# Performance work log

Measured on AMD Instinct MI355X. Metric: run time of the kernel, lower is better.

## Reference

```python
import jax, jax.numpy as jnp
import numpy as np

N = 50000           # num_nodes
E = 400000          # num directed input edges
CON_DIM = 128
STRUC_DIM = 64
HIDDEN = 128
NUM_NODE_UPDATES = 5
MAX_GROUP_ITERS = 100


def setup_inputs() -> dict:
    key = jax.random.key(0)
    k = jax.random.split(key, 5)
    return {
        "con_feats": jax.random.normal(k[0], (N, CON_DIM), jnp.float32),
        "struc_feats": jax.random.normal(k[1], (N, STRUC_DIM), jnp.float32),
        "W1": jax.random.normal(k[2], (2 * CON_DIM, HIDDEN), jnp.float32) * 0.05,
        "b1": jnp.zeros((HIDDEN,), jnp.float32),
        "W2": jax.random.normal(k[3], (HIDDEN, 1), jnp.float32) * 0.05,
        "b2": jnp.zeros((1,), jnp.float32),
        "edge_ids": jax.random.randint(k[4], (2, E), 0, N, jnp.int32),
    }


def _edge_scores(con_feats, W1, b1, W2, b2, src, dst, upper):
    # MLP edge scorer on concatenated endpoint features; relu'd score,
    # zeroed on edges failing the dst > src pruning (equivalent to torch's
    # boolean pruning: score-0 edges contribute nothing downstream).
    x = jnp.concatenate([con_feats[src], con_feats[dst]], axis=1)  # [E, 2*C]
    raw = (jax.nn.relu(x @ W1 + b1) @ W2 + b2)[:, 0]               # [E]
    return jax.nn.relu(raw) * upper


def reference(con_feats, struc_feats, W1, b1, W2, b2, edge_ids):
    num_nodes = con_feats.shape[0]
    src, dst = edge_ids[0], edge_ids[1]
    upper = (dst > src).astype(con_feats.dtype)
    scores = _edge_scores(con_feats, W1, b1, W2, b2, src, dst, upper)
    ar = jnp.arange(num_nodes, dtype=edge_ids.dtype)

    # full edge set: pruned + flipped + self-loops (score-0 edges are no-ops)
    all_src = jnp.concatenate([src, dst, ar])
    all_dst = jnp.concatenate([dst, src, ar])
    all_scores = jnp.concatenate([scores, scores, jnp.ones((num_nodes,), scores.dtype)])

    # row-wise normalization (scatter-sum over source node)
    node_sums = jax.ops.segment_sum(all_scores, all_src, num_segments=num_nodes)
    norm_scores = all_scores / node_sums[all_src]

    def spmm(f):  # sparse [N,N] @ dense [N,d]
        return jax.ops.segment_sum(norm_scores[:, None] * f[all_dst], all_src,
                                   num_segments=num_nodes)

    for _ in range(NUM_NODE_UPDATES):
        con_feats = spmm(con_feats)
        struc_feats = spmm(struc_feats)

    # connected-components label propagation over edges with positive score
    # (edges with score==0 are rewritten as self-edges instead of filtered,
    # which is a no-op for scatter-min; self-loops appended as in torch)
    g_src = jnp.concatenate([jnp.where(scores > 0, src, dst), ar])
    g_dst = jnp.concatenate([dst, ar])

    def cond(state):
        i, _, changed = state
        return (i < MAX_GROUP_ITERS) & changed

    def body(state):
        i, g, _ = state
        new = jax.ops.segment_min(g[g_src], g_dst, num_segments=num_nodes)
        return (i + 1, new, jnp.any(new != g))

    _, group_ids, _ = jax.lax.while_loop(cond, body,
                                         (jnp.int32(0), ar, jnp.bool_(True)))

    # compact labels (torch.unique return_inverse); output padded to N rows
    _, inv = jnp.unique(group_ids, return_inverse=True, size=num_nodes,
                        fill_value=num_nodes - 1)
    inv = inv.reshape(-1)

    counts = jax.ops.segment_sum(jnp.ones((num_nodes,), con_feats.dtype), inv,
                                 num_segments=num_nodes)
    denom = jnp.maximum(counts, 1.0)[:, None]
    con_out = jax.ops.segment_sum(con_feats, inv, num_segments=num_nodes) / denom
    struc_out = jax.ops.segment_sum(struc_feats, inv, num_segments=num_nodes) / denom
    # [N, CON_DIM + STRUC_DIM]; rows >= num_groups are zero padding
    return jnp.concatenate([con_out, struc_out], axis=1)
```

## Files before the change

kernel.cpp:

```cpp
#include <hip/hip_runtime.h>
#include <hip/hip_fp16.h>
#include <cstdint>
#include <cstddef>


__global__ void k_init(const float* __restrict__ con, const float* __restrict__ str,
                       __half* __restrict__ F, float* __restrict__ sums,
                       int* __restrict__ cnt, int* __restrict__ g, int N) {
  int i = blockIdx.x * blockDim.x + threadIdx.x;
  int total = N * 192;
  if (i < total) {
    int n = i / 192, f = i - n * 192;
    float v = (f < 128) ? con[n * 128 + f] : str[n * 64 + (f - 128)];
    F[i] = __float2half_rn(v);
  }
  if (i < N) { sums[i] = 1.0f; cnt[i] = 1; g[i] = i; }
}

__global__ __launch_bounds__(256) void k_proj(const float* __restrict__ con,
                                              const float* __restrict__ W1,
                                              const float* __restrict__ b1,
                                              float* __restrict__ PQf,
                                              __half* __restrict__ PQh, int N) {
  int wave = threadIdx.x >> 6;
  int lane = threadIdx.x & 63;
  int n0 = blockIdx.x * 32 + wave * 8;
  const float* W1q = W1 + 128 * 128;
  float aP0[8], aP1[8], aQ0[8], aQ1[8];
#pragma unroll
  for (int t = 0; t < 8; ++t) { aP0[t] = 0.f; aP1[t] = 0.f; aQ0[t] = 0.f; aQ1[t] = 0.f; }
  int cL = lane, cH = 64 + lane;
  for (int k = 0; k < 128; k += 4) {
    float wP0[4], wP1[4], wQ0[4], wQ1[4];
#pragma unroll
    for (int u = 0; u < 4; ++u) {
      wP0[u] = W1[(k + u) * 128 + cL];
      wP1[u] = W1[(k + u) * 128 + cH];
      wQ0[u] = W1q[(k + u) * 128 + cL];
      wQ1[u] = W1q[(k + u) * 128 + cH];
    }
#pragma unroll
    for (int t = 0; t < 8; ++t) {
      int node = min(n0 + t, N - 1);
      const float4 c4 = *(const float4*)&con[(size_t)node * 128 + k];
      aP0[t] += c4.x * wP0[0] + c4.y * wP0[1] + c4.z * wP0[2] + c4.w * wP0[3];
      aP1[t] += c4.x * wP1[0] + c4.y * wP1[1] + c4.z * wP1[2] + c4.w * wP1[3];
      aQ0[t] += c4.x * wQ0[0] + c4.y * wQ0[1] + c4.z * wQ0[2] + c4.w * wQ0[3];
      aQ1[t] += c4.x * wQ1[0] + c4.y * wQ1[1] + c4.z * wQ1[2] + c4.w * wQ1[3];
    }
  }
  float bL = b1[cL], bH = b1[cH];
#pragma unroll
  for (int t = 0; t < 8; ++t) {
    int node = n0 + t;
    if (node < N) {
      float vP0 = aP0[t] + bL, vP1 = aP1[t] + bH;
      float* rf = PQf + (size_t)node * 256;
      rf[cL] = vP0; rf[cH] = vP1;
      rf[128 + cL] = aQ0[t]; rf[128 + cH] = aQ1[t];
      __half* rh = PQh + (size_t)node * 256;
      rh[cL] = __float2half_rn(vP0); rh[cH] = __float2half_rn(vP1);
      rh[128 + cL] = __float2half_rn(aQ0[t]); rh[128 + cH] = __float2half_rn(aQ1[t]);
    }
  }
}

__global__ __launch_bounds__(256) void k_edge(const int* __restrict__ src, const int* __restrict__ dst,
                                              const __half* __restrict__ PQ,
                                              const float* __restrict__ PQf,
                                              const float* __restrict__ W2,
                                              const float* __restrict__ b2,
                                              float* __restrict__ scores,
                                              float* __restrict__ sums, int* __restrict__ cnt,
                                              int* __restrict__ pos_s, int* __restrict__ pos_d,
                                              int* __restrict__ pos_cnt, int E) {
  int e = blockIdx.x * 256 + threadIdx.x;
  bool live = (e < E);
  int s = 0, d = 0;
  if (live) { s = src[e]; d = dst[e]; }
  bool scored = live && (d > s);
  float raw = -1.0f;
  if (scored) {
    const uint4* P = (const uint4*)(PQ + (size_t)s * 256);
    const uint4* Q = (const uint4*)(PQ + (size_t)d * 256 + 128);
    const float4* W = (const float4*)W2;
    float acc = 0.0f;
#pragma unroll 8
    for (int k = 0; k < 16; ++k) {
      uint4 pu = P[k];
      uint4 qu = Q[k];
      float4 wa = W[2 * k], wb = W[2 * k + 1];
      float2 p0 = __half22float2(*(const __half2*)&pu.x);
      float2 p1 = __half22float2(*(const __half2*)&pu.y);
      float2 p2 = __half22float2(*(const __half2*)&pu.z);
      float2 p3 = __half22float2(*(const __half2*)&pu.w);
      float2 q0 = __half22float2(*(const __half2*)&qu.x);
      float2 q1 = __half22float2(*(const __half2*)&qu.y);
      float2 q2 = __half22float2(*(const __half2*)&qu.z);
      float2 q3 = __half22float2(*(const __half2*)&qu.w);
      acc += fmaxf(p0.x + q0.x, 0.f) * wa.x + fmaxf(p0.y + q0.y, 0.f) * wa.y
           + fmaxf(p1.x + q1.x, 0.f) * wa.z + fmaxf(p1.y + q1.y, 0.f) * wa.w
           + fmaxf(p2.x + q2.x, 0.f) * wb.x + fmaxf(p2.y + q2.y, 0.f) * wb.y
           + fmaxf(p3.x + q3.x, 0.f) * wb.z + fmaxf(p3.y + q3.y, 0.f) * wb.w;
    }
    raw = acc + b2[0];
    if (fabsf(raw) < 3e-3f) {
      const float4* Pf = (const float4*)(PQf + (size_t)s * 256);
      const float4* Qf = (const float4*)(PQf + (size_t)d * 256 + 128);
      float acc2 = 0.0f;
      for (int k = 0; k < 32; ++k) {
        float4 p = Pf[k], q = Qf[k], w = W[k];
        acc2 += fmaxf(p.x + q.x, 0.f) * w.x + fmaxf(p.y + q.y, 0.f) * w.y
              + fmaxf(p.z + q.z, 0.f) * w.z + fmaxf(p.w + q.w, 0.f) * w.w;
      }
      raw = acc2 + b2[0];
    }
  }
  float sc = scored ? fmaxf(raw, 0.0f) : 0.0f;
  if (live) scores[e] = sc;
  bool pos = scored && (sc > 0.0f);
  if (pos) {
    atomicAdd(&sums[s], sc);
    atomicAdd(&sums[d], sc);
    atomicAdd(&cnt[s], 1);
    atomicAdd(&cnt[d], 1);
  }
  unsigned long long m = __ballot(pos);
  if (pos) {
    int lane = threadIdx.x & 63;
    int rank = __popcll(m & ((1ULL << lane) - 1));
    int leader = __ffsll((long long)m) - 1;
    int bcast;
    if (lane == leader) bcast = atomicAdd(pos_cnt, __popcll(m));
    bcast = __shfl(bcast, leader, 64);
    pos_s[bcast + rank] = s;
    pos_d[bcast + rank] = d;
  }
}

__device__ __forceinline__ int wave_iscan(int v) {
  int l = threadIdx.x & 63;
#pragma unroll
  for (int o = 1; o < 64; o <<= 1) {
    int t = __shfl_up(v, o, 64);
    if (l >= o) v += t;
  }
  return v;
}

__global__ __launch_bounds__(1024) void k_scan_red(int mode, const int* __restrict__ cnt,
                                                   const int* __restrict__ g,
                                                   int* __restrict__ bsum, int N) {
  __shared__ int wsum[16];
  int i = blockIdx.x * 1024 + threadIdx.x;
  int v = 0;
  if (i < N) v = (mode == 0) ? cnt[i] : ((g[i] == i) ? 1 : 0);
  int incl = wave_iscan(v);
  int wid = threadIdx.x >> 6;
  if ((threadIdx.x & 63) == 63) wsum[wid] = incl;
  __syncthreads();
  if (threadIdx.x == 0) {
    int t = 0;
#pragma unroll
    for (int k = 0; k < 16; ++k) t += wsum[k];
    bsum[blockIdx.x] = t;
  }
}

__global__ __launch_bounds__(64) void k_scan_mid(int mode, const int* __restrict__ bsum,
                                                 int* __restrict__ bexcl, int NB,
                                                 int* __restrict__ rowp, int N) {
  int l = threadIdx.x;
  int v = (l < NB) ? bsum[l] : 0;
  int incl = wave_iscan(v);
  if (l < NB) bexcl[l] = incl - v;
  if (l == 63 && mode == 0) rowp[N] = incl;
}

__global__ __launch_bounds__(1024) void k_scan_out(int mode, const int* __restrict__ cnt,
                                                   const int* __restrict__ g,
                                                   const float* __restrict__ sums,
                                                   const int* __restrict__ bexcl,
                                                   int* __restrict__ rowp, int* __restrict__ fillp,
                                                   int* __restrict__ col, float* __restrict__ wt,
                                                   int* __restrict__ rank, int N) {
  __shared__ int wsum[16];
  int i = blockIdx.x * 1024 + threadIdx.x;
  int v = 0;
  if (i < N) v = (mode == 0) ? cnt[i] : ((g[i] == i) ? 1 : 0);
  int incl = wave_iscan(v);
  int wid = threadIdx.x >> 6;
  if ((threadIdx.x & 63) == 63) wsum[wid] = incl;
  __syncthreads();
  if (threadIdx.x < 64) {
    int l = threadIdx.x;
    int sv = (l < 16) ? wsum[l] : 0;
#pragma unroll
    for (int o = 1; o < 16; o <<= 1) {
      int t = __shfl_up(sv, o, 64);
      if (l >= o) sv += t;
    }
    if (l < 16) wsum[l] = sv;
  }
  __syncthreads();
  int wexcl = (wid == 0) ? 0 : wsum[wid - 1];
  int excl = bexcl[blockIdx.x] + wexcl + incl - v;
  if (i < N) {
    if (mode == 0) {
      rowp[i] = excl;
      fillp[i] = excl + 1;
      col[excl] = i;
      wt[excl] = 1.0f / sums[i];
    } else {
      rank[i] = excl;
    }
  }
}

__global__ void k_fill(const int* __restrict__ src, const int* __restrict__ dst,
                       const float* __restrict__ scores, const float* __restrict__ sums,
                       int* __restrict__ fillp, int* __restrict__ col, float* __restrict__ wt,
                       int E) {
  int e = blockIdx.x * blockDim.x + threadIdx.x;
  if (e >= E) return;
  float sc = scores[e];
  if (sc <= 0.0f) return;
  int s = src[e], d = dst[e];
  int p = atomicAdd(&fillp[s], 1);
  col[p] = d; wt[p] = sc / sums[s];
  int p2 = atomicAdd(&fillp[d], 1);
  col[p2] = s; wt[p2] = sc / sums[d];
}

__global__ __launch_bounds__(192) void k_spmm(const __half* __restrict__ Fin, __half* __restrict__ Fout,
                                              const int* __restrict__ rowp,
                                              const int* __restrict__ col,
                                              const float* __restrict__ wt, int N) {
  int tid = blockIdx.x * 192 + threadIdx.x;
  int row = tid / 24;
  int f8 = tid - row * 24;
  if (row >= N) return;
  const uint4* F8 = (const uint4*)Fin;
  int beg = rowp[row], end = rowp[row + 1];
  float a0 = 0.f, a1 = 0.f, a2 = 0.f, a3 = 0.f, a4 = 0.f, a5 = 0.f, a6 = 0.f, a7 = 0.f;
  int idx = beg;
  for (; idx + 1 < end; idx += 2) {
    int c0 = col[idx], c1 = col[idx + 1];
    float w0 = wt[idx], w1 = wt[idx + 1];
    uint4 u0 = F8[(size_t)c0 * 24 + f8];
    uint4 u1 = F8[(size_t)c1 * 24 + f8];
    float2 x0 = __half22float2(*(const __half2*)&u0.x);
    float2 x1 = __half22float2(*(const __half2*)&u0.y);
    float2 x2 = __half22float2(*(const __half2*)&u0.z);
    float2 x3 = __half22float2(*(const __half2*)&u0.w);
    a0 += w0 * x0.x; a1 += w0 * x0.y; a2 += w0 * x1.x; a3 += w0 * x1.y;
    a4 += w0 * x2.x; a5 += w0 * x2.y; a6 += w0 * x3.x; a7 += w0 * x3.y;
    float2 y0 = __half22float2(*(const __half2*)&u1.x);
    float2 y1 = __half22float2(*(const __half2*)&u1.y);
    float2 y2 = __half22float2(*(const __half2*)&u1.z);
    float2 y3 = __half22float2(*(const __half2*)&u1.w);
    a0 += w1 * y0.x; a1 += w1 * y0.y; a2 += w1 * y1.x; a3 += w1 * y1.y;
    a4 += w1 * y2.x; a5 += w1 * y2.y; a6 += w1 * y3.x; a7 += w1 * y3.y;
  }
  if (idx < end) {
    int c0 = col[idx];
    float w0 = wt[idx];
    uint4 u0 = F8[(size_t)c0 * 24 + f8];
    float2 x0 = __half22float2(*(const __half2*)&u0.x);
    float2 x1 = __half22float2(*(const __half2*)&u0.y);
    float2 x2 = __half22float2(*(const __half2*)&u0.z);
    float2 x3 = __half22float2(*(const __half2*)&u0.w);
    a0 += w0 * x0.x; a1 += w0 * x0.y; a2 += w0 * x1.x; a3 += w0 * x1.y;
    a4 += w0 * x2.x; a5 += w0 * x2.y; a6 += w0 * x3.x; a7 += w0 * x3.y;
  }
  uint4 o;
  *(__half2*)&o.x = __floats2half2_rn(a0, a1);
  *(__half2*)&o.y = __floats2half2_rn(a2, a3);
  *(__half2*)&o.z = __floats2half2_rn(a4, a5);
  *(__half2*)&o.w = __floats2half2_rn(a6, a7);
  ((uint4*)Fout)[(size_t)row * 24 + f8] = o;
}

__global__ void k_prop(const int* __restrict__ pos_s, const int* __restrict__ pos_d,
                       const int* __restrict__ pos_cnt, int* g, int N) {
  int i = blockIdx.x * blockDim.x + threadIdx.x;
  volatile int* gv = g;
  int P = *pos_cnt;
#pragma unroll
  for (int r = 0; r < 2; ++r) {
    if (i < P) {
      int s = pos_s[i], d = pos_d[i];
      int gs = gv[s];
      if (gs < gv[d]) atomicMin(&g[d], gs);
    }
    if (i < N) {
      int gi = gv[i];
      int gg = gv[gi];
      if (gg < gi) atomicMin(&g[i], gg);
      gi = gv[i];
      gg = gv[gi];
      if (gg < gi) atomicMin(&g[i], gg);
    }
  }
}

__global__ void k_gcnt(const int* __restrict__ g, const int* __restrict__ rank,
                       int* __restrict__ gcnt, int N) {
  int i = blockIdx.x * blockDim.x + threadIdx.x;
  if (i < N) atomicAdd(&gcnt[rank[g[i]]], 1);
}

__global__ void k_inv(const int* __restrict__ gcnt, float* __restrict__ invc, int N) {
  int i = blockIdx.x * blockDim.x + threadIdx.x;
  if (i < N) invc[i] = 1.0f / (float)max(gcnt[i], 1);
}

__global__ __launch_bounds__(192) void k_accum(const __half* __restrict__ F, const int* __restrict__ g,
                                               const int* __restrict__ rank,
                                               const float* __restrict__ invc,
                                               float* __restrict__ out, int N) {
  __shared__ int jbuf[64];
  int n0 = blockIdx.x * 64;
  if (threadIdx.x < 64) {
    int n = n0 + threadIdx.x;
    jbuf[threadIdx.x] = (n < N) ? rank[g[n]] : -1;
  }
  __syncthreads();
  int f = threadIdx.x;
  int lim = min(64, N - n0);
  float acc = 0.0f; int cur = -1;
  for (int k = 0; k < lim; ++k) {
    int j = jbuf[k];
    float v = __half2float(F[(size_t)(n0 + k) * 192 + f]);
    if (j != cur) {
      if (cur >= 0) atomicAdd(&out[(size_t)cur * 192 + f], acc * invc[cur]);
      cur = j; acc = v;
    } else {
      acc += v;
    }
  }
  if (cur >= 0) atomicAdd(&out[(size_t)cur * 192 + f], acc * invc[cur]);
}

extern "C" void kernel_launch(void* const* d_in, const int* in_sizes, int n_in,
                              void* d_out, int out_size, void* d_ws, size_t ws_size,
                              hipStream_t stream) {
  const float* con = (const float*)d_in[0];
  const float* str = (const float*)d_in[1];
  const float* W1  = (const float*)d_in[2];
  const float* b1  = (const float*)d_in[3];
  const float* W2  = (const float*)d_in[4];
  const float* b2  = (const float*)d_in[5];
  const int* edges = (const int*)d_in[6];
  int N = in_sizes[0] / 128;
  int E = in_sizes[6] / 2;
  const int* src = edges;
  const int* dst = edges + E;
  int NB = (N + 1023) / 1024;

  uint8_t* w = (uint8_t*)d_ws;
  size_t off = 0;
  auto alloc = [&](size_t bytes) -> void* {
    void* p = w + off;
    off += (bytes + 255) & ~(size_t)255;
    return p;
  };
  __half* Fa    = (__half*)alloc((size_t)N * 192 * 2);
  float*  PQf   = (float*)alloc((size_t)N * 256 * 4);
  __half* Fb    = (__half*)PQf;
  float* scores = (float*)alloc((size_t)E * 4);
  float* sums   = (float*)alloc((size_t)N * 4);
  int*   cnt    = (int*)alloc((size_t)N * 4);
  int*   g      = (int*)alloc((size_t)N * 4);
  int*   pos_s  = (int*)alloc((size_t)E * 4);
  int*   pos_d  = (int*)alloc((size_t)E * 4);
  int*   pos_c  = (int*)alloc(256);
  int*   bsum   = (int*)alloc(64 * 4);
  int*   bexcl  = (int*)alloc(64 * 4);
  size_t mark = off;
  int*   colA   = (int*)alloc((2 * (size_t)E + N) * 4);
  float* wtA    = (float*)alloc((2 * (size_t)E + N) * 4);
  int*   rowp   = (int*)alloc((size_t)(N + 1) * 4);
  int*   fillp  = (int*)alloc((size_t)N * 4);
  int*   rank   = (int*)alloc((size_t)N * 4);
  int*   gcnt   = (int*)alloc((size_t)N * 4);
  float* invc   = (float*)alloc((size_t)N * 4);
  size_t pqh_bytes = (size_t)N * 256 * 2;
  if (off < mark + pqh_bytes) off = mark + ((pqh_bytes + 255) & ~(size_t)255);
  __half* PQh = (__half*)(w + mark);

  hipMemsetAsync(d_out, 0, (size_t)out_size * 4, stream);
  hipMemsetAsync(pos_c, 0, 4, stream);

  k_init<<<(N * 192 + 255) / 256, 256, 0, stream>>>(con, str, Fa, sums, cnt, g, N);
  k_proj<<<(N + 31) / 32, 256, 0, stream>>>(con, W1, b1, PQf, PQh, N);
  k_edge<<<(E + 255) / 256, 256, 0, stream>>>(src, dst, PQh, PQf, W2, b2, scores, sums, cnt,
                                              pos_s, pos_d, pos_c, E);
  k_scan_red<<<NB, 1024, 0, stream>>>(0, cnt, g, bsum, N);
  k_scan_mid<<<1, 64, 0, stream>>>(0, bsum, bexcl, NB, rowp, N);
  k_scan_out<<<NB, 1024, 0, stream>>>(0, cnt, g, sums, bexcl, rowp, fillp, colA, wtA, rank, N);
  k_fill<<<(E + 255) / 256, 256, 0, stream>>>(src, dst, scores, sums, fillp, colA, wtA, E);

  __half* fin = Fa; __half* fout = Fb;
  for (int it = 0; it < 5; ++it) {
    k_spmm<<<((size_t)N * 24 + 191) / 192, 192, 0, stream>>>(fin, fout, rowp, colA, wtA, N);
    __half* tmp = fin; fin = fout; fout = tmp;
  }

  for (int r = 0; r < 9; ++r)
    k_prop<<<(E + 255) / 256, 256, 0, stream>>>(pos_s, pos_d, pos_c, g, N);

  k_scan_red<<<NB, 1024, 0, stream>>>(1, cnt, g, bsum, N);
  k_scan_mid<<<1, 64, 0, stream>>>(1, bsum, bexcl, NB, rowp, N);
  k_scan_out<<<NB, 1024, 0, stream>>>(1, cnt, g, sums, bexcl, rowp, fillp, colA, wtA, rank, N);
  hipMemsetAsync(gcnt, 0, (size_t)N * 4, stream);
  k_gcnt<<<(N + 255) / 256, 256, 0, stream>>>(g, rank, gcnt, N);
  k_inv<<<(N + 255) / 256, 256, 0, stream>>>(gcnt, invc, N);
  k_accum<<<(N + 63) / 64, 192, 0, stream>>>(fin, g, rank, invc, (float*)d_out, N);
}
```

Before: 588.8 us.

## Compute node projections with fp16 MFMA and rescore borderline edges exactly

Replaces the scalar fp32 per-node W1 projection with an MFMA 16x16x32 fp16 matrix-core kernel over the fp16 feature buffer. A transposed fp16 copy of W1 is prepared first, and the fp32 PQ copy is dropped. Edges whose fp16 score lands near zero are collected into a list. A separate kernel recomputes those from the original fp32 features with a full fp32 MLP. This removes the fp32 projection compute and the extra PQf write and read, at the cost of an extra launch and more slow per-edge recomputes due to the wider border threshold.

```diff
diff --git a/kernel.cpp b/kernel.cpp
--- a/kernel.cpp
+++ b/kernel.cpp
@@ -3,6 +3,9 @@
 #include <cstdint>
 #include <cstddef>
 
+
+typedef _Float16 f16x8 __attribute__((ext_vector_type(8)));
+typedef float f32x4 __attribute__((ext_vector_type(4)));
 
 __global__ void k_init(const float* __restrict__ con, const float* __restrict__ str,
                        __half* __restrict__ F, float* __restrict__ sums,
@@ -17,63 +20,57 @@
   if (i < N) { sums[i] = 1.0f; cnt[i] = 1; g[i] = i; }
 }
 
-__global__ __launch_bounds__(256) void k_proj(const float* __restrict__ con,
-                                              const float* __restrict__ W1,
-                                              const float* __restrict__ b1,
-                                              float* __restrict__ PQf,
-                                              __half* __restrict__ PQh, int N) {
-  int wave = threadIdx.x >> 6;
-  int lane = threadIdx.x & 63;
-  int n0 = blockIdx.x * 32 + wave * 8;
-  const float* W1q = W1 + 128 * 128;
-  float aP0[8], aP1[8], aQ0[8], aQ1[8];
-#pragma unroll
-  for (int t = 0; t < 8; ++t) { aP0[t] = 0.f; aP1[t] = 0.f; aQ0[t] = 0.f; aQ1[t] = 0.f; }
-  int cL = lane, cH = 64 + lane;
-  for (int k = 0; k < 128; k += 4) {
-    float wP0[4], wP1[4], wQ0[4], wQ1[4];
-#pragma unroll
-    for (int u = 0; u < 4; ++u) {
-      wP0[u] = W1[(k + u) * 128 + cL];
-      wP1[u] = W1[(k + u) * 128 + cH];
-      wQ0[u] = W1q[(k + u) * 128 + cL];
-      wQ1[u] = W1q[(k + u) * 128 + cH];
-    }
-#pragma unroll
-    for (int t = 0; t < 8; ++t) {
-      int node = min(n0 + t, N - 1);
-      const float4 c4 = *(const float4*)&con[(size_t)node * 128 + k];
-      aP0[t] += c4.x * wP0[0] + c4.y * wP0[1] + c4.z * wP0[2] + c4.w * wP0[3];
-      aP1[t] += c4.x * wP1[0] + c4.y * wP1[1] + c4.z * wP1[2] + c4.w * wP1[3];
-      aQ0[t] += c4.x * wQ0[0] + c4.y * wQ0[1] + c4.z * wQ0[2] + c4.w * wQ0[3];
-      aQ1[t] += c4.x * wQ1[0] + c4.y * wQ1[1] + c4.z * wQ1[2] + c4.w * wQ1[3];
-    }
-  }
-  float bL = b1[cL], bH = b1[cH];
-#pragma unroll
-  for (int t = 0; t < 8; ++t) {
-    int node = n0 + t;
-    if (node < N) {
-      float vP0 = aP0[t] + bL, vP1 = aP1[t] + bH;
-      float* rf = PQf + (size_t)node * 256;
-      rf[cL] = vP0; rf[cH] = vP1;
-      rf[128 + cL] = aQ0[t]; rf[128 + cH] = aQ1[t];
-      __half* rh = PQh + (size_t)node * 256;
-      rh[cL] = __float2half_rn(vP0); rh[cH] = __float2half_rn(vP1);
-      rh[128 + cL] = __float2half_rn(aQ0[t]); rh[128 + cH] = __float2half_rn(aQ1[t]);
+__global__ void k_wprep(const float* __restrict__ W1, __half* __restrict__ BT) {
+  int i = blockIdx.x * 256 + threadIdx.x;
+  if (i < 256 * 128) {
+    int c = i >> 7, k = i & 127;
+    float v = (c < 128) ? W1[k * 128 + c] : W1[16384 + k * 128 + (c - 128)];
+    BT[(size_t)c * 128 + k] = __float2half_rn(v);
+  }
+}
+
+__global__ __launch_bounds__(256) void k_projm(const __half* __restrict__ Fa,
+                                               const __half* __restrict__ BT,
+                                               const float* __restrict__ b1,
+                                               __half* __restrict__ PQh, int N) {
+  int wave = threadIdx.x >> 6, lane = threadIdx.x & 63;
+  int m0 = blockIdx.x * 16;
+  int r16 = lane & 15, grp = lane >> 4;
+  const _Float16* A = (const _Float16*)Fa;
+  const _Float16* B = (const _Float16*)BT;
+  int node = m0 + r16; if (node >= N) node = N - 1;
+  f16x8 afr[4];
+#pragma unroll
+  for (int ks = 0; ks < 4; ++ks)
+    afr[ks] = *(const f16x8*)(A + (size_t)node * 192 + ks * 32 + grp * 8);
+#pragma unroll
+  for (int nt = 0; nt < 4; ++nt) {
+    int col = (wave * 4 + nt) * 16 + r16;
+    f32x4 acc = {0.f, 0.f, 0.f, 0.f};
+#pragma unroll
+    for (int ks = 0; ks < 4; ++ks) {
+      f16x8 bfr = *(const f16x8*)(B + (size_t)col * 128 + ks * 32 + grp * 8);
+      acc = __builtin_amdgcn_mfma_f32_16x16x32_f16(afr[ks], bfr, acc, 0, 0, 0);
+    }
+    float bias = (col < 128) ? b1[col] : 0.0f;
+#pragma unroll
+    for (int r = 0; r < 4; ++r) {
+      int nrow = m0 + grp * 4 + r;
+      if (nrow < N) PQh[(size_t)nrow * 256 + col] = __float2half_rn(acc[r] + bias);
     }
   }
 }
 
 __global__ __launch_bounds__(256) void k_edge(const int* __restrict__ src, const int* __restrict__ dst,
                                               const __half* __restrict__ PQ,
-                                              const float* __restrict__ PQf,
                                               const float* __restrict__ W2,
                                               const float* __restrict__ b2,
                                               float* __restrict__ scores,
                                               float* __restrict__ sums, int* __restrict__ cnt,
                                               int* __restrict__ pos_s, int* __restrict__ pos_d,
-                                              int* __restrict__ pos_cnt, int E) {
+                                              int* __restrict__ pos_cnt,
+                                              int* __restrict__ bord, int* __restrict__ bord_cnt,
+                                              int E) {
   int e = blockIdx.x * 256 + threadIdx.x;
   bool live = (e < E);
   int s = 0, d = 0;
@@ -104,37 +101,90 @@
            + fmaxf(p3.x + q3.x, 0.f) * wb.z + fmaxf(p3.y + q3.y, 0.f) * wb.w;
     }
     raw = acc + b2[0];
-    if (fabsf(raw) < 3e-3f) {
-      const float4* Pf = (const float4*)(PQf + (size_t)s * 256);
-      const float4* Qf = (const float4*)(PQf + (size_t)d * 256 + 128);
-      float acc2 = 0.0f;
-      for (int k = 0; k < 32; ++k) {
-        float4 p = Pf[k], q = Qf[k], w = W[k];
-        acc2 += fmaxf(p.x + q.x, 0.f) * w.x + fmaxf(p.y + q.y, 0.f) * w.y
-              + fmaxf(p.z + q.z, 0.f) * w.z + fmaxf(p.w + q.w, 0.f) * w.w;
-      }
-      raw = acc2 + b2[0];
-    }
-  }
-  float sc = scored ? fmaxf(raw, 0.0f) : 0.0f;
-  if (live) scores[e] = sc;
-  bool pos = scored && (sc > 0.0f);
+  }
+  bool border = scored && (fabsf(raw) < 1e-2f);
+  bool fin = scored && !border;
+  float sc = fin ? fmaxf(raw, 0.0f) : 0.0f;
+  if (live && !border) scores[e] = sc;
+  bool pos = fin && (sc > 0.0f);
   if (pos) {
     atomicAdd(&sums[s], sc);
     atomicAdd(&sums[d], sc);
     atomicAdd(&cnt[s], 1);
     atomicAdd(&cnt[d], 1);
   }
-  unsigned long long m = __ballot(pos);
-  if (pos) {
-    int lane = threadIdx.x & 63;
-    int rank = __popcll(m & ((1ULL << lane) - 1));
-    int leader = __ffsll((long long)m) - 1;
-    int bcast;
-    if (lane == leader) bcast = atomicAdd(pos_cnt, __popcll(m));
-    bcast = __shfl(bcast, leader, 64);
-    pos_s[bcast + rank] = s;
-    pos_d[bcast + rank] = d;
+  int lane = threadIdx.x & 63;
+  {
+    unsigned long long m = __ballot(pos);
+    if (pos) {
+      int rank = __popcll(m & ((1ULL << lane) - 1));
+      int leader = __ffsll((long long)m) - 1;
+      int bcast;
+      if (lane == leader) bcast = atomicAdd(pos_cnt, __popcll(m));
+      bcast = __shfl(bcast, leader, 64);
+      pos_s[bcast + rank] = s;
+      pos_d[bcast + rank] = d;
+    }
+  }
+  {
+    unsigned long long m = __ballot(border);
+    if (border) {
+      int rank = __popcll(m & ((1ULL << lane) - 1));
+      int leader = __ffsll((long long)m) - 1;
+      int bcast;
+      if (lane == leader) bcast = atomicAdd(bord_cnt, __popcll(m));
+      bcast = __shfl(bcast, leader, 64);
+      bord[bcast + rank] = e;
+    }
+  }
+}
+
+__global__ __launch_bounds__(256) void k_border(const int* __restrict__ src, const int* __restrict__ dst,
+                                                const float* __restrict__ con,
+                                                const float* __restrict__ W1,
+                                                const float* __restrict__ b1,
+                                                const float* __restrict__ W2,
+                                                const float* __restrict__ b2,
+                                                const int* __restrict__ bord,
+                                                const int* __restrict__ bord_cnt,
+                                                float* __restrict__ scores,
+                                                float* __restrict__ sums, int* __restrict__ cnt,
+                                                int* __restrict__ pos_s, int* __restrict__ pos_d,
+                                                int* __restrict__ pos_cnt) {
+  int nb = *bord_cnt;
+  int lane = threadIdx.x & 63;
+  int wid = (blockIdx.x * 256 + threadIdx.x) >> 6;
+  int nwaves = (gridDim.x * 256) >> 6;
+  const float* W1q = W1 + 128 * 128;
+  int j0 = lane, j1 = lane + 64;
+  float b1v0 = b1[j0], b1v1 = b1[j1];
+  float w2v0 = W2[j0], w2v1 = W2[j1];
+  for (int w = wid; w < nb; w += nwaves) {
+    int e = bord[w];
+    int s = src[e], d = dst[e];
+    const float* cs = con + (size_t)s * 128;
+    const float* cd = con + (size_t)d * 128;
+    float h0 = 0.f, h1 = 0.f;
+    for (int k = 0; k < 128; ++k) {
+      float a = cs[k], b = cd[k];
+      h0 += a * W1[k * 128 + j0] + b * W1q[k * 128 + j0];
+      h1 += a * W1[k * 128 + j1] + b * W1q[k * 128 + j1];
+    }
+    float v = fmaxf(h0 + b1v0, 0.f) * w2v0 + fmaxf(h1 + b1v1, 0.f) * w2v1;
+#pragma unroll
+    for (int o = 32; o > 0; o >>= 1) v += __shfl_xor(v, o, 64);
+    if (lane == 0) {
+      float sc = fmaxf(v + b2[0], 0.0f);
+      scores[e] = sc;
+      if (sc > 0.0f) {
+        atomicAdd(&sums[s], sc);
+        atomicAdd(&sums[d], sc);
+        atomicAdd(&cnt[s], 1);
+        atomicAdd(&cnt[d], 1);
+        int p = atomicAdd(pos_cnt, 1);
+        pos_s[p] = s; pos_d[p] = d;
+      }
+    }
   }
 }
 
@@ -366,8 +416,7 @@
     return p;
   };
   __half* Fa    = (__half*)alloc((size_t)N * 192 * 2);
-  float*  PQf   = (float*)alloc((size_t)N * 256 * 4);
-  __half* Fb    = (__half*)PQf;
+  __half* Fb    = (__half*)alloc((size_t)N * 192 * 2);
   float* scores = (float*)alloc((size_t)E * 4);
   float* sums   = (float*)alloc((size_t)N * 4);
   int*   cnt    = (int*)alloc((size_t)N * 4);
@@ -375,6 +424,8 @@
   int*   pos_s  = (int*)alloc((size_t)E * 4);
   int*   pos_d  = (int*)alloc((size_t)E * 4);
   int*   pos_c  = (int*)alloc(256);
+  int*   bord   = (int*)alloc((size_t)E * 4);
+  __half* BT    = (__half*)alloc((size_t)256 * 128 * 2);
   int*   bsum   = (int*)alloc(64 * 4);
   int*   bexcl  = (int*)alloc(64 * 4);
   size_t mark = off;
@@ -390,12 +441,15 @@
   __half* PQh = (__half*)(w + mark);
 
   hipMemsetAsync(d_out, 0, (size_t)out_size * 4, stream);
-  hipMemsetAsync(pos_c, 0, 4, stream);
+  hipMemsetAsync(pos_c, 0, 8, stream);
 
   k_init<<<(N * 192 + 255) / 256, 256, 0, stream>>>(con, str, Fa, sums, cnt, g, N);
-  k_proj<<<(N + 31) / 32, 256, 0, stream>>>(con, W1, b1, PQf, PQh, N);
-  k_edge<<<(E + 255) / 256, 256, 0, stream>>>(src, dst, PQh, PQf, W2, b2, scores, sums, cnt,
-                                              pos_s, pos_d, pos_c, E);
+  k_wprep<<<(256 * 128 + 255) / 256, 256, 0, stream>>>(W1, BT);
+  k_projm<<<(N + 15) / 16, 256, 0, stream>>>(Fa, BT, b1, PQh, N);
+  k_edge<<<(E + 255) / 256, 256, 0, stream>>>(src, dst, PQh, W2, b2, scores, sums, cnt,
+                                              pos_s, pos_d, &pos_c[0], bord, &pos_c[1], E);
+  k_border<<<512, 256, 0, stream>>>(src, dst, con, W1, b1, W2, b2, bord, &pos_c[1],
+                                    scores, sums, cnt, pos_s, pos_d, &pos_c[0]);
   k_scan_red<<<NB, 1024, 0, stream>>>(0, cnt, g, bsum, N);
   k_scan_mid<<<1, 64, 0, stream>>>(0, bsum, bexcl, NB, rowp, N);
   k_scan_out<<<NB, 1024, 0, stream>>>(0, cnt, g, sums, bexcl, rowp, fillp, colA, wtA, rank, N);
@@ -408,7 +462,7 @@
   }
 
   for (int r = 0; r < 9; ++r)
-    k_prop<<<(E + 255) / 256, 256, 0, stream>>>(pos_s, pos_d, pos_c, g, N);
+    k_prop<<<(E + 255) / 256, 256, 0, stream>>>(pos_s, pos_d, &pos_c[0], g, N);
 
   k_scan_red<<<NB, 1024, 0, stream>>>(1, cnt, g, bsum, N);
   k_scan_mid<<<1, 64, 0, stream>>>(1, bsum, bexcl, NB, rowp, N);
```

New measurement: 587.2 us. No clear change (-0.3%).
